# Kernel optimization log

Measured on AMD Instinct MI355X. Metric: run time of the kernel, lower is better.

The kernel has to match this reference:

```python
import jax, jax.numpy as jnp
import numpy as np

B, T, D = 4, 2048, 2048
H, HD = 16, 128          # heads, head_dim (H*HD == D)
I = 5632                 # intermediate size
CAP = 0.25
K = int(T * CAP)         # 512 tokens selected per batch row
S = B * K                # packed sequence length
THETA = 10000.0
EPS = 1e-6


def setup_inputs() -> dict:
    key = jax.random.key(0)
    ks = jax.random.split(key, 12)
    s = 0.02
    w = lambda k, shp: jax.random.normal(k, shp, jnp.float32) * s
    return {
        "hidden_states": jax.random.normal(ks[0], (B, T, D), jnp.float32),
        "router_w": w(ks[1], (D,)),
        "router_b": jnp.zeros((1,), jnp.float32),
        "ln1_w": jnp.ones((D,), jnp.float32),
        "ln2_w": jnp.ones((D,), jnp.float32),
        "wq": w(ks[2], (D, D)), "bq": jnp.zeros((D,), jnp.float32),
        "wk": w(ks[3], (D, D)), "bk": jnp.zeros((D,), jnp.float32),
        "wv": w(ks[4], (D, D)), "bv": jnp.zeros((D,), jnp.float32),
        "wo": w(ks[5], (D, D)),
        "w_gate": w(ks[6], (D, I)),
        "w_up": w(ks[7], (D, I)),
        "w_down": w(ks[8], (I, D)),
    }


def _rms(x, w):
    return x * jax.lax.rsqrt(jnp.mean(x * x, axis=-1, keepdims=True) + EPS) * w


def _rotate_half(x):
    x1, x2 = jnp.split(x, 2, axis=-1)
    return jnp.concatenate([-x2, x1], axis=-1)


def reference(hidden_states, router_w, router_b, ln1_w, ln2_w,
              wq, bq, wk, bk, wv, bv, wo, w_gate, w_up, w_down):
    # ---- router: per-token scalar scores, top-k per batch row ----
    scores = hidden_states @ router_w + router_b[0]          # [B,T]
    _, idx = jax.lax.top_k(scores, K)                        # [B,K]
    idx = jnp.sort(idx, axis=-1)                             # causal order in packed seq

    # ---- gather selected tokens into packed batch-1 sequence ----
    sel = jnp.take_along_axis(hidden_states, idx[..., None], axis=1)  # [B,K,D]
    sel_scores = jnp.take_along_axis(scores, idx, axis=1)             # [B,K]
    x = sel.reshape(S, D)
    pos = idx.reshape(S)                                     # original token positions

    # ---- rotary tables gathered at original positions ----
    inv_freq = 1.0 / (THETA ** (jnp.arange(0, HD, 2, dtype=jnp.float32) / HD))
    freqs = pos.astype(jnp.float32)[:, None] * inv_freq[None, :]      # [S,HD/2]
    emb = jnp.concatenate([freqs, freqs], axis=-1)                    # [S,HD]
    cos, sin = jnp.cos(emb)[:, None, :], jnp.sin(emb)[:, None, :]     # [S,1,HD]

    # ---- Qwen2 decoder block (attention) ----
    h = _rms(x, ln1_w)
    q = (h @ wq + bq).reshape(S, H, HD)
    k = (h @ wk + bk).reshape(S, H, HD)
    v = (h @ wv + bv).reshape(S, H, HD)
    q = q * cos + _rotate_half(q) * sin
    k = k * cos + _rotate_half(k) * sin

    att = jnp.einsum("shd,thd->hst", q, k) / np.sqrt(HD).astype(np.float32)
    causal = jnp.tril(jnp.ones((S, S), bool))
    att = jnp.where(causal[None], att, jnp.finfo(att.dtype).min)
    p = jax.nn.softmax(att, axis=-1)
    attn_out = jnp.einsum("hst,thd->shd", p, v).reshape(S, D) @ wo
    x1 = x + attn_out

    # ---- Qwen2 decoder block (SwiGLU MLP) ----
    h2 = _rms(x1, ln2_w)
    mlp = (jax.nn.silu(h2 @ w_gate) * (h2 @ w_up)) @ w_down
    processed = x1 + mlp                                     # [S,D]

    # ---- sigmoid gate blend + scatter back ----
    gate = jax.nn.sigmoid(sel_scores).reshape(S, 1)
    blended = gate * processed + (1.0 - gate) * x            # [S,D]
    out = hidden_states.at[jnp.arange(B)[:, None], idx].set(blended.reshape(B, K, D))
    return out
```

## Files before the change

### kernel.cpp

```cpp
#include <hip/hip_runtime.h>
#include <stdint.h>

#define B_ 4
#define T_ 2048
#define D_ 2048
#define H_ 16
#define HD_ 128
#define I_ 5632
#define K_ 512
#define S_ 2048
#define D3_ (3 * D_)

typedef float f32x4 __attribute__((ext_vector_type(4)));
typedef short s16x8 __attribute__((ext_vector_type(8)));
typedef __bf16 bf16x8 __attribute__((ext_vector_type(8)));

template <typename V>
__device__ __forceinline__ auto mfma_try(V a, V b, f32x4 c, int)
    -> decltype(__builtin_amdgcn_mfma_f32_16x16x32_bf16(a, b, c, 0, 0, 0)) {
  return __builtin_amdgcn_mfma_f32_16x16x32_bf16(a, b, c, 0, 0, 0);
}
template <typename V>
__device__ __forceinline__ f32x4 mfma_try(V a, V b, f32x4 c, long) {
  return __builtin_amdgcn_mfma_f32_16x16x32_bf16(
      __builtin_bit_cast(bf16x8, a), __builtin_bit_cast(bf16x8, b), c, 0, 0, 0);
}
__device__ __forceinline__ f32x4 mfma_bf16(s16x8 a, s16x8 b, f32x4 c) {
  return mfma_try(a, b, c, 0);
}

__device__ __forceinline__ void gl_lds16(const void* g, void* l) {
  __builtin_amdgcn_global_load_lds((const __attribute__((address_space(1))) void*)g,
                                   (__attribute__((address_space(3))) void*)l, 16, 0, 0);
}

__device__ __forceinline__ unsigned short f2bf(float f) {
  unsigned u = __float_as_uint(f);
  u += 0x7FFFu + ((u >> 16) & 1);
  return (unsigned short)(u >> 16);
}
__device__ __forceinline__ float bf2f(unsigned short s) {
  return __uint_as_float(((unsigned)s) << 16);
}

__global__ __launch_bounds__(256) void k_copy_scores(const float4* __restrict__ hid,
                                                     float4* __restrict__ dst,
                                                     const float4* __restrict__ rw,
                                                     const float* __restrict__ rb,
                                                     float* __restrict__ scores) {
  int row = blockIdx.x, t = threadIdx.x;
  const float4* hr = hid + (size_t)row * (D_ / 4);
  float4* dr = dst + (size_t)row * (D_ / 4);
  float acc = 0.f;
#pragma unroll
  for (int i = 0; i < 2; i++) {
    float4 v = hr[t + i * 256];
    dr[t + i * 256] = v;
    float4 w = rw[t + i * 256];
    acc += v.x * w.x + v.y * w.y + v.z * w.z + v.w * w.w;
  }
#pragma unroll
  for (int d = 32; d; d >>= 1) acc += __shfl_xor(acc, d);
  __shared__ float red[4];
  if ((t & 63) == 0) red[t >> 6] = acc;
  __syncthreads();
  if (t == 0) scores[row] = red[0] + red[1] + red[2] + red[3] + rb[0];
}

__global__ __launch_bounds__(1024) void k_topk(const float* __restrict__ scores,
                                               int* __restrict__ pos) {
  __shared__ unsigned long long keys[T_];
  __shared__ int sidx[K_];
  int b = blockIdx.x, t = threadIdx.x;
  for (int i = t; i < T_; i += 1024) {
    unsigned u = __float_as_uint(scores[b * T_ + i]);
    u = (u & 0x80000000u) ? ~u : (u | 0x80000000u);
    keys[i] = ((unsigned long long)u << 32) | (unsigned)(~(unsigned)i);
  }
  __syncthreads();
  for (int k = 2; k <= T_; k <<= 1)
    for (int j = k >> 1; j > 0; j >>= 1) {
      for (int i = t; i < T_; i += 1024) {
        int l = i ^ j;
        if (l > i) {
          unsigned long long a = keys[i], c = keys[l];
          bool desc = ((i & k) == 0);
          if (desc ? (a < c) : (a > c)) { keys[i] = c; keys[l] = a; }
        }
      }
      __syncthreads();
    }
  if (t < K_) sidx[t] = (int)(~(unsigned)(keys[t] & 0xFFFFFFFFull));
  __syncthreads();
  for (int k = 2; k <= K_; k <<= 1)
    for (int j = k >> 1; j > 0; j >>= 1) {
      if (t < K_) {
        int i = t, l = i ^ j;
        if (l > i && l < K_) {
          int a = sidx[i], c = sidx[l];
          bool asc = ((i & k) == 0);
          if (asc ? (a > c) : (a < c)) { sidx[i] = c; sidx[l] = a; }
        }
      }
      __syncthreads();
    }
  if (t < K_) pos[b * K_ + t] = sidx[t];
}

__global__ __launch_bounds__(256) void k_gather(const float* __restrict__ hidden,
    const int* __restrict__ pos, const float* __restrict__ scores,
    const float* __restrict__ ln1w, float* __restrict__ x,
    unsigned short* __restrict__ xn, float* __restrict__ gate,
    float* __restrict__ cosb, float* __restrict__ sinb) {
  int s = blockIdx.x, t = threadIdx.x;
  int b = s >> 9, p = pos[s];
  const float* src = hidden + ((size_t)b * T_ + p) * D_;
  float v[8];
  float ss = 0.f;
#pragma unroll
  for (int i = 0; i < 8; i++) { v[i] = src[t + i * 256]; ss += v[i] * v[i]; }
  __shared__ float red[4];
#pragma unroll
  for (int d = 32; d; d >>= 1) ss += __shfl_xor(ss, d);
  if ((t & 63) == 0) red[t >> 6] = ss;
  __syncthreads();
  ss = red[0] + red[1] + red[2] + red[3];
  float scale = rsqrtf(ss / (float)D_ + 1e-6f);
  float* xd = x + (size_t)s * D_;
  unsigned short* xnd = xn + (size_t)s * D_;
#pragma unroll
  for (int i = 0; i < 8; i++) {
    int c = t + i * 256;
    xd[c] = v[i];
    xnd[c] = f2bf(v[i] * scale * ln1w[c]);
  }
  if (t == 0) gate[s] = 1.f / (1.f + expf(-scores[b * T_ + p]));
  if (t < 64) {
    float invf = powf(10000.0f, -(float)t / 64.0f);
    float f = (float)p * invf;
    cosb[s * 64 + t] = cosf(f);
    sinb[s * 64 + t] = sinf(f);
  }
}

__global__ __launch_bounds__(256) void k_transpose(const float* __restrict__ src,
                                                   unsigned short* __restrict__ dst,
                                                   int R, int C) {
  __shared__ float tile[32][33];
  int tx = threadIdx.x & 31, ty = threadIdx.x >> 5;
  int c0 = blockIdx.x * 32, r0 = blockIdx.y * 32;
#pragma unroll
  for (int i = 0; i < 4; i++) {
    int r = ty + i * 8;
    tile[r][tx] = src[(size_t)(r0 + r) * C + c0 + tx];
  }
  __syncthreads();
#pragma unroll
  for (int i = 0; i < 4; i++) {
    int r = ty + i * 8;
    dst[(size_t)(c0 + r) * R + r0 + tx] = f2bf(tile[tx][r]);
  }
}

#define SWZ(row) ((((row) >> 1) & 3) << 4)

__device__ __forceinline__ void stage16k(const unsigned short* __restrict__ g, int ldK,
                                         int row0, int k0, char* lds, int tid) {
#pragma unroll
  for (int c = 0; c < 2; c++) {
    int off = c * 8192 + tid * 16;
    int row = off >> 6;
    int cb = (off & 63) ^ SWZ(row);
    gl_lds16(g + (size_t)(row0 + row) * ldK + k0 + (cb >> 1), lds + off);
  }
}
__device__ __forceinline__ void stage8k(const unsigned short* __restrict__ g, int ldK,
                                        int row0, int k0, char* lds, int tid) {
  int off = tid * 16;
  int row = off >> 6;
  int cb = (off & 63) ^ SWZ(row);
  gl_lds16(g + (size_t)(row0 + row) * ldK + k0 + (cb >> 1), lds + off);
}
__device__ __forceinline__ void stage64r(const unsigned short* __restrict__ g, int ldK,
                                         int row0, int k0, char* lds, int tid) {
  int off = tid * 16;
  int row = off >> 6;
  int cb = (off & 63) ^ SWZ(row);
  gl_lds16(g + (size_t)(row0 + row) * ldK + k0 + (cb >> 1), lds + off);
}
__device__ __forceinline__ void stage128r(const unsigned short* __restrict__ g, int ldK,
                                          int row0, int k0, char* lds, int tid) {
#pragma unroll
  for (int c = 0; c < 2; c++) {
    int off = c * 4096 + tid * 16;
    int row = off >> 6;
    int cb = (off & 63) ^ SWZ(row);
    gl_lds16(g + (size_t)(row0 + row) * ldK + k0 + (cb >> 1), lds + off);
  }
}
__device__ __forceinline__ s16x8 ldfrag(const char* base, int row, int g) {
  return *(const s16x8*)(base + row * 64 + ((g * 16) ^ SWZ(row)));
}

__global__ __launch_bounds__(512, 2) void k_gemm_qkv8(const unsigned short* __restrict__ A,
    const unsigned short* __restrict__ Bt, unsigned short* __restrict__ C,
    const float* __restrict__ bq, const float* __restrict__ bk,
    const float* __restrict__ bv) {
  alignas(16) __shared__ short As[2][256 * 32];
  alignas(16) __shared__ short Bs[2][128 * 32];
  int tid = threadIdx.x;
  int lane = tid & 63, g = lane >> 4, lr = lane & 15;
  int wid = tid >> 6, wm = wid >> 1, wn = wid & 1;
  int m0 = blockIdx.x * 256, n0 = blockIdx.y * 128;
  f32x4 zero4 = {0.f, 0.f, 0.f, 0.f};
  f32x4 acc[4][4];
#pragma unroll
  for (int m = 0; m < 4; m++)
#pragma unroll
    for (int n = 0; n < 4; n++) acc[m][n] = zero4;
  const int nkt = D_ / 32;
  stage16k(A, D_, m0, 0, (char*)As[0], tid);
  stage8k(Bt, D_, n0, 0, (char*)Bs[0], tid);
  stage16k(A, D_, m0, 32, (char*)As[1], tid);
  stage8k(Bt, D_, n0, 32, (char*)Bs[1], tid);
  int arow = wm * 64 + lr;
  int brow = wn * 64 + lr;
  for (int t = 0; t < nkt; t++) {
    int b = t & 1;
    const char* Ab = (const char*)As[b];
    const char* Bb = (const char*)Bs[b];
    if (t + 1 < nkt) asm volatile("s_waitcnt vmcnt(3)" ::: "memory");
    else             asm volatile("s_waitcnt vmcnt(0)" ::: "memory");
    __builtin_amdgcn_s_barrier();
    s16x8 af[4], bf4[4];
#pragma unroll
    for (int i = 0; i < 4; i++) af[i] = ldfrag(Ab, arow + i * 16, g);
#pragma unroll
    for (int i = 0; i < 4; i++) bf4[i] = ldfrag(Bb, brow + i * 16, g);
    asm volatile("s_waitcnt lgkmcnt(0)" ::: "memory");
    __builtin_amdgcn_s_barrier();
    if (t + 2 < nkt) {
      stage16k(A, D_, m0, (t + 2) * 32, (char*)As[b], tid);
      stage8k(Bt, D_, n0, (t + 2) * 32, (char*)Bs[b], tid);
    }
    __builtin_amdgcn_s_setprio(1);
#pragma unroll
    for (int m = 0; m < 4; m++)
#pragma unroll
      for (int n = 0; n < 4; n++) acc[m][n] = mfma_bf16(af[m], bf4[n], acc[m][n]);
    __builtin_amdgcn_s_setprio(0);
  }
#pragma unroll
  for (int m = 0; m < 4; m++)
#pragma unroll
    for (int n = 0; n < 4; n++)
#pragma unroll
      for (int r = 0; r < 4; r++) {
        int row = m0 + wm * 64 + m * 16 + (g << 2) + r;
        int col = n0 + wn * 64 + n * 16 + lr;
        float bias = (col < D_) ? bq[col] : ((col < 2 * D_) ? bk[col - D_] : bv[col - 2 * D_]);
        C[(size_t)row * D3_ + col] = f2bf(acc[m][n][r] + bias);
      }
}

__global__ __launch_bounds__(512, 2) void k_gemm_gup8(const unsigned short* __restrict__ A,
    const unsigned short* __restrict__ Bg, const unsigned short* __restrict__ Bu,
    unsigned short* __restrict__ act) {
  alignas(16) __shared__ short As[2][256 * 32];
  alignas(16) __shared__ short Bgs[2][128 * 32];
  alignas(16) __shared__ short Bus[2][128 * 32];
  int tid = threadIdx.x;
  int lane = tid & 63, g = lane >> 4, lr = lane & 15;
  int wid = tid >> 6, wm = wid >> 1, wn = wid & 1;
  int m0 = blockIdx.x * 256, n0 = blockIdx.y * 128;
  f32x4 zero4 = {0.f, 0.f, 0.f, 0.f};
  f32x4 ag[4][4], au[4][4];
#pragma unroll
  for (int m = 0; m < 4; m++)
#pragma unroll
    for (int n = 0; n < 4; n++) { ag[m][n] = zero4; au[m][n] = zero4; }
  const int nkt = D_ / 32;
  stage16k(A, D_, m0, 0, (char*)As[0], tid);
  stage8k(Bg, D_, n0, 0, (char*)Bgs[0], tid);
  stage8k(Bu, D_, n0, 0, (char*)Bus[0], tid);
  stage16k(A, D_, m0, 32, (char*)As[1], tid);
  stage8k(Bg, D_, n0, 32, (char*)Bgs[1], tid);
  stage8k(Bu, D_, n0, 32, (char*)Bus[1], tid);
  int arow = wm * 64 + lr;
  int brow = wn * 64 + lr;
  for (int t = 0; t < nkt; t++) {
    int b = t & 1;
    const char* Ab = (const char*)As[b];
    const char* Bgb = (const char*)Bgs[b];
    const char* Bub = (const char*)Bus[b];
    if (t + 1 < nkt) asm volatile("s_waitcnt vmcnt(4)" ::: "memory");
    else             asm volatile("s_waitcnt vmcnt(0)" ::: "memory");
    __builtin_amdgcn_s_barrier();
    s16x8 af[4], bg4[4], bu4[4];
#pragma unroll
    for (int i = 0; i < 4; i++) af[i] = ldfrag(Ab, arow + i * 16, g);
#pragma unroll
    for (int i = 0; i < 4; i++) bg4[i] = ldfrag(Bgb, brow + i * 16, g);
#pragma unroll
    for (int i = 0; i < 4; i++) bu4[i] = ldfrag(Bub, brow + i * 16, g);
    asm volatile("s_waitcnt lgkmcnt(0)" ::: "memory");
    __builtin_amdgcn_s_barrier();
    if (t + 2 < nkt) {
      stage16k(A, D_, m0, (t + 2) * 32, (char*)As[b], tid);
      stage8k(Bg, D_, n0, (t + 2) * 32, (char*)Bgs[b], tid);
      stage8k(Bu, D_, n0, (t + 2) * 32, (char*)Bus[b], tid);
    }
    __builtin_amdgcn_s_setprio(1);
#pragma unroll
    for (int m = 0; m < 4; m++)
#pragma unroll
      for (int n = 0; n < 4; n++) {
        ag[m][n] = mfma_bf16(af[m], bg4[n], ag[m][n]);
        au[m][n] = mfma_bf16(af[m], bu4[n], au[m][n]);
      }
    __builtin_amdgcn_s_setprio(0);
  }
#pragma unroll
  for (int m = 0; m < 4; m++)
#pragma unroll
    for (int n = 0; n < 4; n++)
#pragma unroll
      for (int r = 0; r < 4; r++) {
        int row = m0 + wm * 64 + m * 16 + (g << 2) + r;
        int col = n0 + wn * 64 + n * 16 + lr;
        float gv = ag[m][n][r], uv = au[m][n][r];
        float si = gv / (1.f + __expf(-gv));
        act[(size_t)row * I_ + col] = f2bf(si * uv);
      }
}

__global__ __launch_bounds__(256, 2) void k_gemm_wo64(const unsigned short* __restrict__ A,
    const unsigned short* __restrict__ Bt, const float* __restrict__ xres,
    float* __restrict__ x1) {
  alignas(16) __shared__ short As[2][64 * 32];
  alignas(16) __shared__ short Bs[2][128 * 32];
  int tid = threadIdx.x;
  int lane = tid & 63, g = lane >> 4, lr = lane & 15, wid = tid >> 6;
  int m0 = blockIdx.x * 64, n0 = blockIdx.y * 128;
  f32x4 zero4 = {0.f, 0.f, 0.f, 0.f};
  f32x4 acc[4][2];
#pragma unroll
  for (int m = 0; m < 4; m++)
#pragma unroll
    for (int n = 0; n < 2; n++) acc[m][n] = zero4;
  const int nkt = D_ / 32;
  stage64r(A, D_, m0, 0, (char*)As[0], tid);
  stage128r(Bt, D_, n0, 0, (char*)Bs[0], tid);
  stage64r(A, D_, m0, 32, (char*)As[1], tid);
  stage128r(Bt, D_, n0, 32, (char*)Bs[1], tid);
  for (int t = 0; t < nkt; t++) {
    int b = t & 1;
    const char* Ab = (const char*)As[b];
    const char* Bb = (const char*)Bs[b];
    if (t + 1 < nkt) asm volatile("s_waitcnt vmcnt(3)" ::: "memory");
    else             asm volatile("s_waitcnt vmcnt(0)" ::: "memory");
    __builtin_amdgcn_s_barrier();
    s16x8 af[4], bf2[2];
#pragma unroll
    for (int i = 0; i < 4; i++) af[i] = ldfrag(Ab, i * 16 + lr, g);
#pragma unroll
    for (int j = 0; j < 2; j++) bf2[j] = ldfrag(Bb, wid * 32 + j * 16 + lr, g);
    asm volatile("s_waitcnt lgkmcnt(0)" ::: "memory");
    __builtin_amdgcn_s_barrier();
    if (t + 2 < nkt) {
      stage64r(A, D_, m0, (t + 2) * 32, (char*)As[b], tid);
      stage128r(Bt, D_, n0, (t + 2) * 32, (char*)Bs[b], tid);
    }
    __builtin_amdgcn_s_setprio(1);
#pragma unroll
    for (int m = 0; m < 4; m++)
#pragma unroll
      for (int n = 0; n < 2; n++) acc[m][n] = mfma_bf16(af[m], bf2[n], acc[m][n]);
    __builtin_amdgcn_s_setprio(0);
  }
#pragma unroll
  for (int m = 0; m < 4; m++)
#pragma unroll
    for (int n = 0; n < 2; n++)
#pragma unroll
      for (int r = 0; r < 4; r++) {
        int row = m0 + m * 16 + (g << 2) + r;
        int col = n0 + wid * 32 + n * 16 + lr;
        x1[(size_t)row * D_ + col] = acc[m][n][r] + xres[(size_t)row * D_ + col];
      }
}

__global__ __launch_bounds__(256, 2) void k_gemm_down64(const unsigned short* __restrict__ A,
    const unsigned short* __restrict__ Bt, const float* __restrict__ x1,
    const float* __restrict__ x, const float* __restrict__ gate,
    const int* __restrict__ pos, float* __restrict__ out) {
  alignas(16) __shared__ short As[2][64 * 32];
  alignas(16) __shared__ short Bs[2][128 * 32];
  int tid = threadIdx.x;
  int lane = tid & 63, g = lane >> 4, lr = lane & 15, wid = tid >> 6;
  int m0 = blockIdx.x * 64, n0 = blockIdx.y * 128;
  f32x4 zero4 = {0.f, 0.f, 0.f, 0.f};
  f32x4 acc[4][2];
#pragma unroll
  for (int m = 0; m < 4; m++)
#pragma unroll
    for (int n = 0; n < 2; n++) acc[m][n] = zero4;
  const int nkt = I_ / 32;
  stage64r(A, I_, m0, 0, (char*)As[0], tid);
  stage128r(Bt, I_, n0, 0, (char*)Bs[0], tid);
  stage64r(A, I_, m0, 32, (char*)As[1], tid);
  stage128r(Bt, I_, n0, 32, (char*)Bs[1], tid);
  for (int t = 0; t < nkt; t++) {
    int b = t & 1;
    const char* Ab = (const char*)As[b];
    const char* Bb = (const char*)Bs[b];
    if (t + 1 < nkt) asm volatile("s_waitcnt vmcnt(3)" ::: "memory");
    else             asm volatile("s_waitcnt vmcnt(0)" ::: "memory");
    __builtin_amdgcn_s_barrier();
    s16x8 af[4], bf2[2];
#pragma unroll
    for (int i = 0; i < 4; i++) af[i] = ldfrag(Ab, i * 16 + lr, g);
#pragma unroll
    for (int j = 0; j < 2; j++) bf2[j] = ldfrag(Bb, wid * 32 + j * 16 + lr, g);
    asm volatile("s_waitcnt lgkmcnt(0)" ::: "memory");
    __builtin_amdgcn_s_barrier();
    if (t + 2 < nkt) {
      stage64r(A, I_, m0, (t + 2) * 32, (char*)As[b], tid);
      stage128r(Bt, I_, n0, (t + 2) * 32, (char*)Bs[b], tid);
    }
    __builtin_amdgcn_s_setprio(1);
#pragma unroll
    for (int m = 0; m < 4; m++)
#pragma unroll
      for (int n = 0; n < 2; n++) acc[m][n] = mfma_bf16(af[m], bf2[n], acc[m][n]);
    __builtin_amdgcn_s_setprio(0);
  }
#pragma unroll
  for (int m = 0; m < 4; m++)
#pragma unroll
    for (int n = 0; n < 2; n++)
#pragma unroll
      for (int r = 0; r < 4; r++) {
        int srow = m0 + m * 16 + (g << 2) + r;
        int col = n0 + wid * 32 + n * 16 + lr;
        float proc = acc[m][n][r] + x1[(size_t)srow * D_ + col];
        float gt = gate[srow];
        float xv = x[(size_t)srow * D_ + col];
        int bb = srow >> 9;
        int p = pos[srow];
        out[((size_t)bb * T_ + p) * D_ + col] = gt * proc + (1.f - gt) * xv;
      }
}

__global__ __launch_bounds__(256) void k_rope(const unsigned short* __restrict__ qkv,
    const float* __restrict__ cosb, const float* __restrict__ sinb,
    unsigned short* __restrict__ qh, unsigned short* __restrict__ kh,
    unsigned short* __restrict__ vT) {
  int s0 = blockIdx.x * 64;
  int h = blockIdx.y;
  int t = threadIdx.x;
#pragma unroll
  for (int i = 0; i < 16; i++) {
    int flat = t + i * 256;
    int r = flat >> 6, dp = flat & 63;
    int s = s0 + r;
    float c = cosb[s * 64 + dp], sn = sinb[s * 64 + dp];
    const unsigned short* qrow = qkv + (size_t)s * D3_ + h * HD_;
    float q1 = bf2f(qrow[dp]), q2 = bf2f(qrow[dp + 64]);
    unsigned short* qdst = qh + ((size_t)h * S_ + s) * HD_;
    qdst[dp] = f2bf(q1 * c - q2 * sn);
    qdst[dp + 64] = f2bf(q2 * c + q1 * sn);
    const unsigned short* krow = qrow + D_;
    float k1 = bf2f(krow[dp]), k2 = bf2f(krow[dp + 64]);
    unsigned short* kdst = kh + ((size_t)h * S_ + s) * HD_;
    kdst[dp] = f2bf(k1 * c - k2 * sn);
    kdst[dp + 64] = f2bf(k2 * c + k1 * sn);
  }
  __shared__ unsigned short vt[128][66];
#pragma unroll
  for (int i = 0; i < 32; i++) {
    int flat = t + i * 256;
    int r = flat >> 7, d = flat & 127;
    vt[d][r] = qkv[(size_t)(s0 + r) * D3_ + 2 * D_ + h * HD_ + d];
  }
  __syncthreads();
#pragma unroll
  for (int i = 0; i < 32; i++) {
    int flat = t + i * 256;
    int d = flat >> 6, sc = flat & 63;
    vT[((size_t)h * HD_ + d) * S_ + s0 + sc] = vt[d][sc];
  }
}

__device__ __forceinline__ void stage_kv(const unsigned short* __restrict__ kh,
                                         const unsigned short* __restrict__ vT,
                                         size_t hbase, int kt, char* KsB, char* VsB, int tid) {
#pragma unroll
  for (int c = 0; c < 4; c++) {
    int off = c * 4096 + tid * 16;
    int row = off >> 8;
    int cb = (off & 255) ^ ((row & 7) << 4);
    gl_lds16(kh + hbase + (size_t)(kt * 64 + row) * HD_ + (cb >> 1), KsB + off);
  }
#pragma unroll
  for (int c = 0; c < 4; c++) {
    int off = c * 4096 + tid * 16;
    int row = off >> 7;
    int cb = (off & 127) ^ ((row & 7) << 4);
    gl_lds16(vT + hbase + (size_t)row * S_ + kt * 64 + (cb >> 1), VsB + off);
  }
}

__global__ __launch_bounds__(256, 2) void k_attn(const unsigned short* __restrict__ qh,
                                                 const unsigned short* __restrict__ kh,
                                                 const unsigned short* __restrict__ vT,
                                                 unsigned short* __restrict__ ao) {
  alignas(16) __shared__ short Ks[2][64 * 128];
  alignas(16) __shared__ short Vs[2][128 * 64];
  alignas(16) __shared__ short Ps[4][16 * 64];
  int bidx = blockIdx.x;
  int head = bidx & 15;
  int slot = bidx >> 4;
  int qt = (slot < 16) ? (31 - slot) : (slot - 16);
  int q0 = qt * 64;
  int tid = threadIdx.x, w = tid >> 6, lane = tid & 63, g = lane >> 4, lr = lane & 15;
  size_t hbase = (size_t)head * S_ * HD_;
  int qw = q0 + w * 16;
  char* PsW = (char*)&Ps[w][0];
  s16x8 qf[4];
#pragma unroll
  for (int ks = 0; ks < 4; ks++)
    qf[ks] = *(const s16x8*)&qh[hbase + (size_t)(qw + lr) * HD_ + ks * 32 + g * 8];
  f32x4 o[8];
  f32x4 zero4 = {0.f, 0.f, 0.f, 0.f};
#pragma unroll
  for (int nf = 0; nf < 8; nf++) o[nf] = zero4;
  float m_i[4], l_i[4];
#pragma unroll
  for (int r = 0; r < 4; r++) { m_i[r] = -1e30f; l_i[r] = 0.f; }
  const float sc = 0.08838834764831843f;

  stage_kv(kh, vT, hbase, 0, (char*)Ks[0], (char*)Vs[0], tid);
  if (qt > 0) stage_kv(kh, vT, hbase, 1, (char*)Ks[1], (char*)Vs[1], tid);

  for (int kt = 0; kt <= qt; kt++) {
    int b = kt & 1;
    const char* KsB = (const char*)Ks[b];
    const char* VsB = (const char*)Vs[b];
    if (kt < qt) asm volatile("s_waitcnt vmcnt(8)" ::: "memory");
    else         asm volatile("s_waitcnt vmcnt(0)" ::: "memory");
    __builtin_amdgcn_s_barrier();
    f32x4 sacc[4];
#pragma unroll
    for (int nf = 0; nf < 4; nf++) sacc[nf] = zero4;
#pragma unroll
    for (int ks = 0; ks < 4; ks++) {
      s16x8 kf[4];
#pragma unroll
      for (int nf = 0; nf < 4; nf++) {
        int row = nf * 16 + lr;
        kf[nf] = *(const s16x8*)(KsB + row * 256 + (((ks << 6) + (g << 4)) ^ ((row & 7) << 4)));
      }
#pragma unroll
      for (int nf = 0; nf < 4; nf++) sacc[nf] = mfma_bf16(qf[ks], kf[nf], sacc[nf]);
    }
    bool diag = (kt == qt);
#pragma unroll
    for (int r = 0; r < 4; r++) {
      int prow = (g << 2) + r;
      int qrow = qw + prow;
      float pv[4];
      float mx = -1e30f;
#pragma unroll
      for (int nf = 0; nf < 4; nf++) {
        float vv = sacc[nf][r] * sc;
        if (diag) {
          int kc = kt * 64 + nf * 16 + lr;
          vv = (kc <= qrow) ? vv : -1e30f;
        }
        pv[nf] = vv;
        mx = fmaxf(mx, vv);
      }
#pragma unroll
      for (int d = 1; d < 16; d <<= 1) mx = fmaxf(mx, __shfl_xor(mx, d));
      float mold = m_i[r], mnew = fmaxf(mold, mx);
      float corr = __expf(mold - mnew);
      float ssum = 0.f;
#pragma unroll
      for (int nf = 0; nf < 4; nf++) {
        float pe = __expf(pv[nf] - mnew);
        int cb = ((nf * 16 + lr) << 1) ^ ((prow & 7) << 4);
        *(unsigned short*)(PsW + prow * 128 + cb) = f2bf(pe);
        ssum += pe;
      }
#pragma unroll
      for (int d = 1; d < 16; d <<= 1) ssum += __shfl_xor(ssum, d);
      l_i[r] = l_i[r] * corr + ssum;
      m_i[r] = mnew;
#pragma unroll
      for (int nf = 0; nf < 8; nf++) o[nf][r] *= corr;
    }
    s16x8 pa[2];
#pragma unroll
    for (int ks = 0; ks < 2; ks++)
      pa[ks] = *(const s16x8*)(PsW + lr * 128 + (((ks << 6) + (g << 4)) ^ ((lr & 7) << 4)));
#pragma unroll
    for (int nf = 0; nf < 8; nf++) {
#pragma unroll
      for (int ks = 0; ks < 2; ks++) {
        int row = nf * 16 + lr;
        s16x8 vb = *(const s16x8*)(VsB + row * 128 + (((ks << 6) + (g << 4)) ^ ((row & 7) << 4)));
        o[nf] = mfma_bf16(pa[ks], vb, o[nf]);
      }
    }
    asm volatile("s_waitcnt lgkmcnt(0)" ::: "memory");
    __builtin_amdgcn_s_barrier();
    if (kt + 2 <= qt)
      stage_kv(kh, vT, hbase, kt + 2, (char*)Ks[b], (char*)Vs[b], tid);
  }
#pragma unroll
  for (int nf = 0; nf < 8; nf++)
#pragma unroll
    for (int r = 0; r < 4; r++) {
      int row = qw + (g << 2) + r;
      int col = head * HD_ + nf * 16 + lr;
      ao[(size_t)row * D_ + col] = f2bf(o[nf][r] / l_i[r]);
    }
}

__global__ __launch_bounds__(256) void k_rms2(const float* __restrict__ x1,
                                              const float* __restrict__ ln2w,
                                              unsigned short* __restrict__ xn2) {
  int s = blockIdx.x, t = threadIdx.x;
  const float* src = x1 + (size_t)s * D_;
  float v[8];
  float ss = 0.f;
#pragma unroll
  for (int i = 0; i < 8; i++) { v[i] = src[t + i * 256]; ss += v[i] * v[i]; }
  __shared__ float red[4];
#pragma unroll
  for (int d = 32; d; d >>= 1) ss += __shfl_xor(ss, d);
  if ((t & 63) == 0) red[t >> 6] = ss;
  __syncthreads();
  ss = red[0] + red[1] + red[2] + red[3];
  float scale = rsqrtf(ss / (float)D_ + 1e-6f);
  unsigned short* dst = xn2 + (size_t)s * D_;
#pragma unroll
  for (int i = 0; i < 8; i++) {
    int c = t + i * 256;
    dst[c] = f2bf(v[i] * scale * ln2w[c]);
  }
}

extern "C" void kernel_launch(void* const* d_in, const int* in_sizes, int n_in,
                              void* d_out, int out_size, void* d_ws, size_t ws_size,
                              hipStream_t stream) {
  (void)in_sizes; (void)n_in; (void)out_size; (void)ws_size;
  const float* hidden = (const float*)d_in[0];
  const float* router_w = (const float*)d_in[1];
  const float* router_b = (const float*)d_in[2];
  const float* ln1w = (const float*)d_in[3];
  const float* ln2w = (const float*)d_in[4];
  const float* wq = (const float*)d_in[5];
  const float* bq = (const float*)d_in[6];
  const float* wk = (const float*)d_in[7];
  const float* bk = (const float*)d_in[8];
  const float* wv = (const float*)d_in[9];
  const float* bv = (const float*)d_in[10];
  const float* wo = (const float*)d_in[11];
  const float* wg = (const float*)d_in[12];
  const float* wu = (const float*)d_in[13];
  const float* wd = (const float*)d_in[14];
  float* out = (float*)d_out;

  char* ws = (char*)d_ws;
  size_t off = 0;
  auto alloc = [&](size_t bytes) {
    char* p = ws + off;
    off += (bytes + 255) & ~(size_t)255;
    return p;
  };
  unsigned short* wqkvT = (unsigned short*)alloc(3ull * D_ * D_ * 2);
  unsigned short* woT = (unsigned short*)alloc((size_t)D_ * D_ * 2);
  unsigned short* wgT = (unsigned short*)alloc((size_t)I_ * D_ * 2);
  unsigned short* wuT = (unsigned short*)alloc((size_t)I_ * D_ * 2);
  unsigned short* wdT = (unsigned short*)alloc((size_t)D_ * I_ * 2);
  float* scores = (float*)alloc((size_t)B_ * T_ * 4);
  int* pos = (int*)alloc((size_t)S_ * 4);
  float* gate = (float*)alloc((size_t)S_ * 4);
  float* x = (float*)alloc((size_t)S_ * D_ * 4);
  float* x1 = (float*)alloc((size_t)S_ * D_ * 4);
  unsigned short* xn = (unsigned short*)alloc((size_t)S_ * D_ * 2);
  float* cosb = (float*)alloc((size_t)S_ * 64 * 4);
  float* sinb = (float*)alloc((size_t)S_ * 64 * 4);
  unsigned short* qkv = (unsigned short*)alloc((size_t)S_ * D3_ * 2);
  unsigned short* qh = (unsigned short*)alloc((size_t)H_ * S_ * HD_ * 2);
  unsigned short* kh = (unsigned short*)alloc((size_t)H_ * S_ * HD_ * 2);
  unsigned short* vT = (unsigned short*)alloc((size_t)H_ * S_ * HD_ * 2);
  unsigned short* ao = (unsigned short*)alloc((size_t)S_ * D_ * 2);

  k_copy_scores<<<B_ * T_, 256, 0, stream>>>((const float4*)hidden, (float4*)out,
                                             (const float4*)router_w, router_b, scores);

  k_transpose<<<dim3(D_ / 32, D_ / 32), 256, 0, stream>>>(wq, wqkvT, D_, D_);
  k_transpose<<<dim3(D_ / 32, D_ / 32), 256, 0, stream>>>(wk, wqkvT + (size_t)D_ * D_, D_, D_);
  k_transpose<<<dim3(D_ / 32, D_ / 32), 256, 0, stream>>>(wv, wqkvT + 2ull * D_ * D_, D_, D_);
  k_transpose<<<dim3(D_ / 32, D_ / 32), 256, 0, stream>>>(wo, woT, D_, D_);
  k_transpose<<<dim3(I_ / 32, D_ / 32), 256, 0, stream>>>(wg, wgT, D_, I_);
  k_transpose<<<dim3(I_ / 32, D_ / 32), 256, 0, stream>>>(wu, wuT, D_, I_);
  k_transpose<<<dim3(D_ / 32, I_ / 32), 256, 0, stream>>>(wd, wdT, I_, D_);

  k_topk<<<B_, 1024, 0, stream>>>(scores, pos);
  k_gather<<<S_, 256, 0, stream>>>(hidden, pos, scores, ln1w, x, xn, gate, cosb, sinb);

  k_gemm_qkv8<<<dim3(S_ / 256, D3_ / 128), 512, 0, stream>>>(xn, wqkvT, qkv, bq, bk, bv);
  k_rope<<<dim3(S_ / 64, H_), 256, 0, stream>>>(qkv, cosb, sinb, qh, kh, vT);
  k_attn<<<32 * H_, 256, 0, stream>>>(qh, kh, vT, ao);
  k_gemm_wo64<<<dim3(S_ / 64, D_ / 128), 256, 0, stream>>>(ao, woT, x, x1);
  k_rms2<<<S_, 256, 0, stream>>>(x1, ln2w, xn);
  k_gemm_gup8<<<dim3(S_ / 256, I_ / 128), 512, 0, stream>>>(xn, wgT, wuT, qkv);
  k_gemm_down64<<<dim3(S_ / 64, D_ / 128), 256, 0, stream>>>(qkv, wdT, x1, x, gate, pos, out);
}
```

Measured before the change: 566.9 us.

## Enlarge wo/down GEMM tiles, move MFMAs before barrier, vectorize transpose stores

The wo and down-projection GEMMs go from 64x128 to 128x128 block tiles with a 2x2 warp layout, so each warp computes a 64x64 sub-tile. This raises arithmetic intensity but halves the grid, which is now 256 blocks. In the qkv, gate/up, wo and down GEMMs the MFMA loop now runs before the LDS-wait barrier and the next-stage prefetch, overlapping compute with fragment loads. The weight transpose kernel now writes ushort4 vectors instead of scalar stores. The risks are fewer blocks than CUs being awkward and more register pressure under the new launch bound of 3.

```diff
diff --git a/kernel.cpp b/kernel.cpp
--- a/kernel.cpp
+++ b/kernel.cpp
@@ -155,11 +155,14 @@
     tile[r][tx] = src[(size_t)(r0 + r) * C + c0 + tx];
   }
   __syncthreads();
-#pragma unroll
-  for (int i = 0; i < 4; i++) {
-    int r = ty + i * 8;
-    dst[(size_t)(c0 + r) * R + r0 + tx] = f2bf(tile[tx][r]);
-  }
+  int drow = threadIdx.x >> 3;
+  int dc4 = (threadIdx.x & 7) * 4;
+  ushort4 v;
+  v.x = f2bf(tile[dc4 + 0][drow]);
+  v.y = f2bf(tile[dc4 + 1][drow]);
+  v.z = f2bf(tile[dc4 + 2][drow]);
+  v.w = f2bf(tile[dc4 + 3][drow]);
+  *(ushort4*)&dst[(size_t)(c0 + drow) * R + r0 + dc4] = v;
 }
 
 #define SWZ(row) ((((row) >> 1) & 3) << 4)
@@ -176,13 +179,6 @@
 }
 __device__ __forceinline__ void stage8k(const unsigned short* __restrict__ g, int ldK,
                                         int row0, int k0, char* lds, int tid) {
-  int off = tid * 16;
-  int row = off >> 6;
-  int cb = (off & 63) ^ SWZ(row);
-  gl_lds16(g + (size_t)(row0 + row) * ldK + k0 + (cb >> 1), lds + off);
-}
-__device__ __forceinline__ void stage64r(const unsigned short* __restrict__ g, int ldK,
-                                         int row0, int k0, char* lds, int tid) {
   int off = tid * 16;
   int row = off >> 6;
   int cb = (off & 63) ^ SWZ(row);
@@ -237,18 +233,18 @@
     for (int i = 0; i < 4; i++) af[i] = ldfrag(Ab, arow + i * 16, g);
 #pragma unroll
     for (int i = 0; i < 4; i++) bf4[i] = ldfrag(Bb, brow + i * 16, g);
+    __builtin_amdgcn_s_setprio(1);
+#pragma unroll
+    for (int m = 0; m < 4; m++)
+#pragma unroll
+      for (int n = 0; n < 4; n++) acc[m][n] = mfma_bf16(af[m], bf4[n], acc[m][n]);
+    __builtin_amdgcn_s_setprio(0);
     asm volatile("s_waitcnt lgkmcnt(0)" ::: "memory");
     __builtin_amdgcn_s_barrier();
     if (t + 2 < nkt) {
       stage16k(A, D_, m0, (t + 2) * 32, (char*)As[b], tid);
       stage8k(Bt, D_, n0, (t + 2) * 32, (char*)Bs[b], tid);
     }
-    __builtin_amdgcn_s_setprio(1);
-#pragma unroll
-    for (int m = 0; m < 4; m++)
-#pragma unroll
-      for (int n = 0; n < 4; n++) acc[m][n] = mfma_bf16(af[m], bf4[n], acc[m][n]);
-    __builtin_amdgcn_s_setprio(0);
   }
 #pragma unroll
   for (int m = 0; m < 4; m++)
@@ -303,6 +299,15 @@
     for (int i = 0; i < 4; i++) bg4[i] = ldfrag(Bgb, brow + i * 16, g);
 #pragma unroll
     for (int i = 0; i < 4; i++) bu4[i] = ldfrag(Bub, brow + i * 16, g);
+    __builtin_amdgcn_s_setprio(1);
+#pragma unroll
+    for (int m = 0; m < 4; m++)
+#pragma unroll
+      for (int n = 0; n < 4; n++) {
+        ag[m][n] = mfma_bf16(af[m], bg4[n], ag[m][n]);
+        au[m][n] = mfma_bf16(af[m], bu4[n], au[m][n]);
+      }
+    __builtin_amdgcn_s_setprio(0);
     asm volatile("s_waitcnt lgkmcnt(0)" ::: "memory");
     __builtin_amdgcn_s_barrier();
     if (t + 2 < nkt) {
@@ -310,15 +315,6 @@
       stage8k(Bg, D_, n0, (t + 2) * 32, (char*)Bgs[b], tid);
       stage8k(Bu, D_, n0, (t + 2) * 32, (char*)Bus[b], tid);
     }
-    __builtin_amdgcn_s_setprio(1);
-#pragma unroll
-    for (int m = 0; m < 4; m++)
-#pragma unroll
-      for (int n = 0; n < 4; n++) {
-        ag[m][n] = mfma_bf16(af[m], bg4[n], ag[m][n]);
-        au[m][n] = mfma_bf16(af[m], bu4[n], au[m][n]);
-      }
-    __builtin_amdgcn_s_setprio(0);
   }
 #pragma unroll
   for (int m = 0; m < 4; m++)
@@ -334,115 +330,119 @@
       }
 }
 
-__global__ __launch_bounds__(256, 2) void k_gemm_wo64(const unsigned short* __restrict__ A,
+__global__ __launch_bounds__(256, 3) void k_gemm_wo128(const unsigned short* __restrict__ A,
     const unsigned short* __restrict__ Bt, const float* __restrict__ xres,
     float* __restrict__ x1) {
-  alignas(16) __shared__ short As[2][64 * 32];
+  alignas(16) __shared__ short As[2][128 * 32];
   alignas(16) __shared__ short Bs[2][128 * 32];
   int tid = threadIdx.x;
-  int lane = tid & 63, g = lane >> 4, lr = lane & 15, wid = tid >> 6;
-  int m0 = blockIdx.x * 64, n0 = blockIdx.y * 128;
+  int lane = tid & 63, g = lane >> 4, lr = lane & 15;
+  int w = tid >> 6;
+  int wr = (w >> 1) * 64, wc = (w & 1) * 64;
+  int m0 = blockIdx.x * 128, n0 = blockIdx.y * 128;
   f32x4 zero4 = {0.f, 0.f, 0.f, 0.f};
-  f32x4 acc[4][2];
+  f32x4 acc[4][4];
 #pragma unroll
   for (int m = 0; m < 4; m++)
 #pragma unroll
-    for (int n = 0; n < 2; n++) acc[m][n] = zero4;
+    for (int n = 0; n < 4; n++) acc[m][n] = zero4;
   const int nkt = D_ / 32;
-  stage64r(A, D_, m0, 0, (char*)As[0], tid);
+  stage128r(A, D_, m0, 0, (char*)As[0], tid);
   stage128r(Bt, D_, n0, 0, (char*)Bs[0], tid);
-  stage64r(A, D_, m0, 32, (char*)As[1], tid);
+  stage128r(A, D_, m0, 32, (char*)As[1], tid);
   stage128r(Bt, D_, n0, 32, (char*)Bs[1], tid);
   for (int t = 0; t < nkt; t++) {
     int b = t & 1;
     const char* Ab = (const char*)As[b];
     const char* Bb = (const char*)Bs[b];
-    if (t + 1 < nkt) asm volatile("s_waitcnt vmcnt(3)" ::: "memory");
+    if (t + 1 < nkt) asm volatile("s_waitcnt vmcnt(4)" ::: "memory");
     else             asm volatile("s_waitcnt vmcnt(0)" ::: "memory");
     __builtin_amdgcn_s_barrier();
-    s16x8 af[4], bf2[2];
-#pragma unroll
-    for (int i = 0; i < 4; i++) af[i] = ldfrag(Ab, i * 16 + lr, g);
-#pragma unroll
-    for (int j = 0; j < 2; j++) bf2[j] = ldfrag(Bb, wid * 32 + j * 16 + lr, g);
+    s16x8 af[4], bf4[4];
+#pragma unroll
+    for (int i = 0; i < 4; i++) af[i] = ldfrag(Ab, wr + i * 16 + lr, g);
+#pragma unroll
+    for (int i = 0; i < 4; i++) bf4[i] = ldfrag(Bb, wc + i * 16 + lr, g);
+    __builtin_amdgcn_s_setprio(1);
+#pragma unroll
+    for (int m = 0; m < 4; m++)
+#pragma unroll
+      for (int n = 0; n < 4; n++) acc[m][n] = mfma_bf16(af[m], bf4[n], acc[m][n]);
+    __builtin_amdgcn_s_setprio(0);
     asm volatile("s_waitcnt lgkmcnt(0)" ::: "memory");
     __builtin_amdgcn_s_barrier();
     if (t + 2 < nkt) {
-      stage64r(A, D_, m0, (t + 2) * 32, (char*)As[b], tid);
+      stage128r(A, D_, m0, (t + 2) * 32, (char*)As[b], tid);
       stage128r(Bt, D_, n0, (t + 2) * 32, (char*)Bs[b], tid);
     }
-    __builtin_amdgcn_s_setprio(1);
-#pragma unroll
-    for (int m = 0; m < 4; m++)
-#pragma unroll
-      for (int n = 0; n < 2; n++) acc[m][n] = mfma_bf16(af[m], bf2[n], acc[m][n]);
-    __builtin_amdgcn_s_setprio(0);
   }
 #pragma unroll
   for (int m = 0; m < 4; m++)
 #pragma unroll
-    for (int n = 0; n < 2; n++)
+    for (int n = 0; n < 4; n++)
 #pragma unroll
       for (int r = 0; r < 4; r++) {
-        int row = m0 + m * 16 + (g << 2) + r;
-        int col = n0 + wid * 32 + n * 16 + lr;
+        int row = m0 + wr + m * 16 + (g << 2) + r;
+        int col = n0 + wc + n * 16 + lr;
         x1[(size_t)row * D_ + col] = acc[m][n][r] + xres[(size_t)row * D_ + col];
       }
 }
 
-__global__ __launch_bounds__(256, 2) void k_gemm_down64(const unsigned short* __restrict__ A,
+__global__ __launch_bounds__(256, 3) void k_gemm_down128(const unsigned short* __restrict__ A,
     const unsigned short* __restrict__ Bt, const float* __restrict__ x1,
     const float* __restrict__ x, const float* __restrict__ gate,
     const int* __restrict__ pos, float* __restrict__ out) {
-  alignas(16) __shared__ short As[2][64 * 32];
+  alignas(16) __shared__ short As[2][128 * 32];
   alignas(16) __shared__ short Bs[2][128 * 32];
   int tid = threadIdx.x;
-  int lane = tid & 63, g = lane >> 4, lr = lane & 15, wid = tid >> 6;
-  int m0 = blockIdx.x * 64, n0 = blockIdx.y * 128;
+  int lane = tid & 63, g = lane >> 4, lr = lane & 15;
+  int w = tid >> 6;
+  int wr = (w >> 1) * 64, wc = (w & 1) * 64;
+  int m0 = blockIdx.x * 128, n0 = blockIdx.y * 128;
   f32x4 zero4 = {0.f, 0.f, 0.f, 0.f};
-  f32x4 acc[4][2];
+  f32x4 acc[4][4];
 #pragma unroll
   for (int m = 0; m < 4; m++)
 #pragma unroll
-    for (int n = 0; n < 2; n++) acc[m][n] = zero4;
+    for (int n = 0; n < 4; n++) acc[m][n] = zero4;
   const int nkt = I_ / 32;
-  stage64r(A, I_, m0, 0, (char*)As[0], tid);
+  stage128r(A, I_, m0, 0, (char*)As[0], tid);
   stage128r(Bt, I_, n0, 0, (char*)Bs[0], tid);
-  stage64r(A, I_, m0, 32, (char*)As[1], tid);
+  stage128r(A, I_, m0, 32, (char*)As[1], tid);
   stage128r(Bt, I_, n0, 32, (char*)Bs[1], tid);
   for (int t = 0; t < nkt; t++) {
     int b = t & 1;
     const char* Ab = (const char*)As[b];
     const char* Bb = (const char*)Bs[b];
-    if (t + 1 < nkt) asm volatile("s_waitcnt vmcnt(3)" ::: "memory");
+    if (t + 1 < nkt) asm volatile("s_waitcnt vmcnt(4)" ::: "memory");
     else             asm volatile("s_waitcnt vmcnt(0)" ::: "memory");
     __builtin_amdgcn_s_barrier();
-    s16x8 af[4], bf2[2];
-#pragma unroll
-    for (int i = 0; i < 4; i++) af[i] = ldfrag(Ab, i * 16 + lr, g);
-#pragma unroll
-    for (int j = 0; j < 2; j++) bf2[j] = ldfrag(Bb, wid * 32 + j * 16 + lr, g);
+    s16x8 af[4], bf4[4];
+#pragma unroll
+    for (int i = 0; i < 4; i++) af[i] = ldfrag(Ab, wr + i * 16 + lr, g);
+#pragma unroll
+    for (int i = 0; i < 4; i++) bf4[i] = ldfrag(Bb, wc + i * 16 + lr, g);
+    __builtin_amdgcn_s_setprio(1);
+#pragma unroll
+    for (int m = 0; m < 4; m++)
+#pragma unroll
+      for (int n = 0; n < 4; n++) acc[m][n] = mfma_bf16(af[m], bf4[n], acc[m][n]);
+    __builtin_amdgcn_s_setprio(0);
     asm volatile("s_waitcnt lgkmcnt(0)" ::: "memory");
     __builtin_amdgcn_s_barrier();
     if (t + 2 < nkt) {
-      stage64r(A, I_, m0, (t + 2) * 32, (char*)As[b], tid);
+      stage128r(A, I_, m0, (t + 2) * 32, (char*)As[b], tid);
       stage128r(Bt, I_, n0, (t + 2) * 32, (char*)Bs[b], tid);
     }
-    __builtin_amdgcn_s_setprio(1);
-#pragma unroll
-    for (int m = 0; m < 4; m++)
-#pragma unroll
-      for (int n = 0; n < 2; n++) acc[m][n] = mfma_bf16(af[m], bf2[n], acc[m][n]);
-    __builtin_amdgcn_s_setprio(0);
   }
 #pragma unroll
   for (int m = 0; m < 4; m++)
 #pragma unroll
-    for (int n = 0; n < 2; n++)
+    for (int n = 0; n < 4; n++)
 #pragma unroll
       for (int r = 0; r < 4; r++) {
-        int srow = m0 + m * 16 + (g << 2) + r;
-        int col = n0 + wid * 32 + n * 16 + lr;
+        int srow = m0 + wr + m * 16 + (g << 2) + r;
+        int col = n0 + wc + n * 16 + lr;
         float proc = acc[m][n][r] + x1[(size_t)srow * D_ + col];
         float gt = gate[srow];
         float xv = x[(size_t)srow * D_ + col];
@@ -716,8 +716,8 @@
   k_gemm_qkv8<<<dim3(S_ / 256, D3_ / 128), 512, 0, stream>>>(xn, wqkvT, qkv, bq, bk, bv);
   k_rope<<<dim3(S_ / 64, H_), 256, 0, stream>>>(qkv, cosb, sinb, qh, kh, vT);
   k_attn<<<32 * H_, 256, 0, stream>>>(qh, kh, vT, ao);
-  k_gemm_wo64<<<dim3(S_ / 64, D_ / 128), 256, 0, stream>>>(ao, woT, x, x1);
+  k_gemm_wo128<<<dim3(S_ / 128, D_ / 128), 256, 0, stream>>>(ao, woT, x, x1);
   k_rms2<<<S_, 256, 0, stream>>>(x1, ln2w, xn);
   k_gemm_gup8<<<dim3(S_ / 256, I_ / 128), 512, 0, stream>>>(xn, wgT, wuT, qkv);
-  k_gemm_down64<<<dim3(S_ / 64, D_ / 128), 256, 0, stream>>>(qkv, wdT, x1, x, gate, pos, out);
-}
+  k_gemm_down128<<<dim3(S_ / 128, D_ / 128), 256, 0, stream>>>(qkv, wdT, x1, x, gate, pos, out);
+}
```

Result: slower. 619.0 us (+9.2%).
